# Kernel tuning notes

Hardware: AMD Instinct MI355X
Metric: run time of the kernel (lower is better)

The kernel has to match this reference:

```python
import jax, jax.numpy as jnp
import numpy as np

N_NODES = 100000
N_EDGES = 1600000
D_FEAT = 48
N_LAYERS = 3  # GCN(n_layers=3) builds exactly 3 GraphConv layers


def setup_inputs() -> dict:
    key = jax.random.key(0)
    k1, k2, k3 = jax.random.split(key, 3)
    features = jax.random.normal(k1, (N_NODES, D_FEAT), dtype=jnp.float32)
    src = jax.random.randint(k2, (N_EDGES,), 0, N_NODES, dtype=jnp.int32)
    dst = jax.random.randint(k3, (N_EDGES,), 0, N_NODES, dtype=jnp.int32)
    return {"features": features, "src": src, "dst": dst}


def reference(features, src, dst):
    # GraphConv(norm='none', weight=False, bias=False): h_v = sum_{u->v} h_u, then activation.
    # Layers 0..N_LAYERS-2 apply relu; the final layer has no activation.
    h = features
    for i in range(N_LAYERS):
        msgs = h[src]  # gather source features per edge: [E, D]
        h = jax.ops.segment_sum(msgs, dst, num_segments=N_NODES)  # scatter-add to dst
        if i < N_LAYERS - 1:
            h = jax.nn.relu(h)
    return h
```

## Files before the change

kernel.cpp:

```cpp
#include <hip/hip_runtime.h>

#define D 48
#define BSH 8
#define BN 256
#define NBMAX 400
#define CH 256
#define CAPT 5120


__global__ void k_hist(const int* __restrict__ dst, int* __restrict__ histg,
                       int E, int NB, int CHE) {
    int c = blockIdx.x;
    int t = threadIdx.x;
    __shared__ int h[NBMAX];
    for (int b = t; b < NB; b += blockDim.x) h[b] = 0;
    __syncthreads();
    int lo = c * CHE, hi = min(lo + CHE, E);
    for (int i = lo + t; i < hi; i += blockDim.x)
        atomicAdd(&h[dst[i] >> BSH], 1);
    __syncthreads();
    for (int b = t; b < NB; b += blockDim.x) histg[c * NB + b] = h[b];
}

__global__ void k_vscan(const int* __restrict__ histg, int* __restrict__ cbase,
                        int* __restrict__ btot, int NB) {
    int b = blockIdx.x;
    int t = threadIdx.x;
    __shared__ int sh[CH];
    int v = histg[t * NB + b];
    sh[t] = v;
    __syncthreads();
    for (int off = 1; off < CH; off <<= 1) {
        int u = (t >= off) ? sh[t - off] : 0;
        __syncthreads();
        sh[t] += u;
        __syncthreads();
    }
    cbase[t * NB + b] = sh[t] - v;
    if (t == CH - 1) btot[b] = sh[t];
}

__global__ void k_bscan(const int* __restrict__ btot, int* __restrict__ bbase,
                        int* __restrict__ row_ptr, int NB, int N, int E) {
    __shared__ int sh[256];
    __shared__ int srun;
    int t = threadIdx.x;
    if (t == 0) srun = 0;
    __syncthreads();
    int nch = (NB + 255) / 256;
    for (int c = 0; c < nch; c++) {
        int b = c * 256 + t;
        int v = (b < NB) ? btot[b] : 0;
        sh[t] = v;
        __syncthreads();
        for (int off = 1; off < 256; off <<= 1) {
            int u = (t >= off) ? sh[t - off] : 0;
            __syncthreads();
            sh[t] += u;
            __syncthreads();
        }
        int run = srun;
        if (b < NB) bbase[b] = run + sh[t] - v;
        __syncthreads();
        if (t == 255) srun = run + sh[255];
        __syncthreads();
    }
    if (t == 0) { bbase[NB] = E; row_ptr[N] = E; }
}

__global__ void k_scatter(const int* __restrict__ src, const int* __restrict__ dst,
                          const int* __restrict__ bbase, const int* __restrict__ cbase,
                          int* __restrict__ stage, int E, int NB, int CHE) {
    int c = blockIdx.x;
    int t = threadIdx.x;
    __shared__ int cur[NBMAX];
    for (int b = t; b < NB; b += blockDim.x)
        cur[b] = bbase[b] + cbase[c * NB + b];
    __syncthreads();
    int lo = c * CHE, hi = min(lo + CHE, E);
    for (int i = lo + t; i < hi; i += blockDim.x) {
        int s = src[i], d = dst[i];
        int p = atomicAdd(&cur[d >> BSH], 1);
        stage[p] = ((d & (BN - 1)) << 17) | s;
    }
}

__global__ void k_build(const int* __restrict__ stage, const int* __restrict__ bbase,
                        int* __restrict__ row_ptr, int* __restrict__ esrc,
                        int N, int NB) {
    int b = blockIdx.x;
    int t = threadIdx.x;
    __shared__ int lbuf[CAPT];
    __shared__ int lout[CAPT];
    __shared__ int hist[BN];
    __shared__ int cur[BN];
    __shared__ int sh[BN];
    int base = bbase[b];
    int cnt = min(bbase[b + 1] - base, CAPT);
    hist[t] = 0;
    __syncthreads();
    for (int i = t; i < cnt; i += 256) {
        int v = stage[base + i];
        lbuf[i] = v;
        atomicAdd(&hist[v >> 17], 1);
    }
    __syncthreads();
    int orig = hist[t];
    sh[t] = orig;
    __syncthreads();
    for (int off = 1; off < 256; off <<= 1) {
        int u = (t >= off) ? sh[t - off] : 0;
        __syncthreads();
        sh[t] += u;
        __syncthreads();
    }
    int excl = sh[t] - orig;
    cur[t] = excl;
    int node = (b << BSH) + t;
    if (node < N) row_ptr[node] = base + excl;
    __syncthreads();
    for (int i = t; i < cnt; i += 256) {
        int v = lbuf[i];
        int p = atomicAdd(&cur[v >> 17], 1);
        lout[p] = v & 0x1FFFF;
    }
    __syncthreads();
    for (int i = t; i < cnt; i += 256) esrc[base + i] = lout[i];
}


static __device__ inline unsigned int f2bf_rne(float x) {
    unsigned int u = __float_as_uint(x);
    return (u + 0x7FFFu + ((u >> 16) & 1u)) >> 16;
}
static __device__ inline unsigned int pack2(float lo, float hi) {
    return f2bf_rne(lo) | (f2bf_rne(hi) << 16);
}
static __device__ inline float bf_lo(unsigned int u) { return __uint_as_float(u << 16); }
static __device__ inline float bf_hi(unsigned int u) { return __uint_as_float(u & 0xFFFF0000u); }

__global__ void k_cvt(const float* __restrict__ in, unsigned int* __restrict__ out, int n4) {
    int i = blockIdx.x * 256 + threadIdx.x;
    if (i >= n4) return;
    float4 v = ((const float4*)in)[i];
    ((uint2*)out)[i] = make_uint2(pack2(v.x, v.y), pack2(v.z, v.w));
}


template <int RELU, int OUTF32>
__global__ void k_pull(const unsigned int* __restrict__ hin, void* __restrict__ hout,
                       const int* __restrict__ row_ptr, const int* __restrict__ esrc,
                       int n) {
    int grp = threadIdx.x >> 3;
    int lane = threadIdx.x & 7;
    int node = blockIdx.x * 32 + grp;
    if (node >= n) return;
    int jb = row_ptr[node], je = row_ptr[node + 1];
    float a0 = 0.f, a1 = 0.f, a2 = 0.f, a3 = 0.f, a4 = 0.f, a5 = 0.f;
    int j = jb;
    int je8 = jb + ((je - jb) & ~7);
    for (; j < je8; j += 8) {
        int s[8];
#pragma unroll
        for (int u = 0; u < 8; u++) s[u] = esrc[j + u];
        uint2 q[8];
        unsigned int w[8];
#pragma unroll
        for (int u = 0; u < 8; u++) {
            const unsigned int* r = hin + s[u] * 24;
            q[u] = *(const uint2*)(r + 2 * lane);
            w[u] = r[16 + lane];
        }
#pragma unroll
        for (int u = 0; u < 8; u++) {
            a0 += bf_lo(q[u].x); a1 += bf_hi(q[u].x);
            a2 += bf_lo(q[u].y); a3 += bf_hi(q[u].y);
            a4 += bf_lo(w[u]);   a5 += bf_hi(w[u]);
        }
    }
    if (j < je) {
        int rem = je - j;
        int s[7];
#pragma unroll
        for (int u = 0; u < 7; u++) s[u] = (u < rem) ? esrc[j + u] : s[0];
        uint2 q[7];
        unsigned int w[7];
#pragma unroll
        for (int u = 0; u < 7; u++) {
            const unsigned int* r = hin + s[u] * 24;
            if (u < rem) {
                q[u] = *(const uint2*)(r + 2 * lane);
                w[u] = r[16 + lane];
            }
        }
#pragma unroll
        for (int u = 0; u < 7; u++) {
            if (u < rem) {
                a0 += bf_lo(q[u].x); a1 += bf_hi(q[u].x);
                a2 += bf_lo(q[u].y); a3 += bf_hi(q[u].y);
                a4 += bf_lo(w[u]);   a5 += bf_hi(w[u]);
            }
        }
    }
    if (RELU) {
        a0 = fmaxf(a0, 0.f); a1 = fmaxf(a1, 0.f); a2 = fmaxf(a2, 0.f);
        a3 = fmaxf(a3, 0.f); a4 = fmaxf(a4, 0.f); a5 = fmaxf(a5, 0.f);
    }
    if (OUTF32) {
        float* o = (float*)hout + (size_t)node * D;
        *(float4*)(o + 4 * lane) = make_float4(a0, a1, a2, a3);
        *(float2*)(o + 32 + 2 * lane) = make_float2(a4, a5);
    } else {
        unsigned int* o = (unsigned int*)hout + node * 24;
        *(uint2*)(o + 2 * lane) = make_uint2(pack2(a0, a1), pack2(a2, a3));
        o[16 + lane] = pack2(a4, a5);
    }
}

extern "C" void kernel_launch(void* const* d_in, const int* in_sizes, int n_in,
                              void* d_out, int out_size, void* d_ws, size_t ws_size,
                              hipStream_t stream) {
    const float* feat = (const float*)d_in[0];
    const int* src = (const int*)d_in[1];
    const int* dst = (const int*)d_in[2];
    int N = in_sizes[0] / D;
    int E = in_sizes[1];
    int NB = (N + BN - 1) >> BSH;
    int CHE = (E + CH - 1) / CH;

    char* ws = (char*)d_ws;
    int*   histg   = (int*)(ws + ((size_t)0 << 10));
    int*   cbase   = (int*)(ws + ((size_t)512 << 10));
    int*   btot    = (int*)(ws + ((size_t)1024 << 10));
    int*   bbase   = (int*)(ws + ((size_t)1088 << 10));
    int*   row_ptr = (int*)(ws + ((size_t)2048 << 10));
    int*   esrc    = (int*)(ws + ((size_t)3 << 20));
    int*   stage   = (int*)(ws + ((size_t)10 << 20));
    unsigned int* featb = (unsigned int*)(ws + ((size_t)17 << 20));
    unsigned int* hb0   = (unsigned int*)(ws + ((size_t)27 << 20));

    k_hist<<<CH, 1024, 0, stream>>>(dst, histg, E, NB, CHE);
    k_vscan<<<NB, CH, 0, stream>>>(histg, cbase, btot, NB);
    k_bscan<<<1, 256, 0, stream>>>(btot, bbase, row_ptr, NB, N, E);
    k_scatter<<<CH, 1024, 0, stream>>>(src, dst, bbase, cbase, stage, E, NB, CHE);
    k_build<<<NB, 256, 0, stream>>>(stage, bbase, row_ptr, esrc, N, NB);

    int n4 = N * D / 4;
    k_cvt<<<(n4 + 255) / 256, 256, 0, stream>>>(feat, featb, n4);

    int pg = (N + 31) / 32;
    k_pull<1, 0><<<pg, 256, 0, stream>>>(featb, hb0, row_ptr, esrc, N);
    k_pull<1, 0><<<pg, 256, 0, stream>>>(hb0, featb, row_ptr, esrc, N);
    k_pull<0, 1><<<pg, 256, 0, stream>>>(featb, d_out, row_ptr, esrc, N);
}
```

Before: 213.5 us.

## Fuse histogram/scan/convert front end and degree-sort nodes within buckets for pull

Merges the per-chunk histogram and the vertical scan into one kernel that uses global atomics on bucket totals to hand out chunk offsets, and runs the bf16 feature conversion in extra blocks of the same launch. k_build additionally counting-sorts the nodes of each 256-node bucket by in-degree class into a perm array, and the pull kernels process nodes in that order so that groups in a wavefront see similar edge counts. The masked remainder block is replaced with a simple scalar loop. The goal is fewer launches and less divergence in the gather; the cost is an extra memset and indirection, plus chunk offsets that are no longer ordered by chunk, which still yields a correct CSR.

```diff
diff --git a/kernel.cpp b/kernel.cpp
--- a/kernel.cpp
+++ b/kernel.cpp
@@ -8,37 +8,41 @@
 #define CAPT 5120
 
 
-__global__ void k_hist(const int* __restrict__ dst, int* __restrict__ histg,
-                       int E, int NB, int CHE) {
-    int c = blockIdx.x;
-    int t = threadIdx.x;
-    __shared__ int h[NBMAX];
-    for (int b = t; b < NB; b += blockDim.x) h[b] = 0;
-    __syncthreads();
-    int lo = c * CHE, hi = min(lo + CHE, E);
-    for (int i = lo + t; i < hi; i += blockDim.x)
-        atomicAdd(&h[dst[i] >> BSH], 1);
-    __syncthreads();
-    for (int b = t; b < NB; b += blockDim.x) histg[c * NB + b] = h[b];
-}
-
-__global__ void k_vscan(const int* __restrict__ histg, int* __restrict__ cbase,
-                        int* __restrict__ btot, int NB) {
-    int b = blockIdx.x;
-    int t = threadIdx.x;
-    __shared__ int sh[CH];
-    int v = histg[t * NB + b];
-    sh[t] = v;
-    __syncthreads();
-    for (int off = 1; off < CH; off <<= 1) {
-        int u = (t >= off) ? sh[t - off] : 0;
-        __syncthreads();
-        sh[t] += u;
-        __syncthreads();
-    }
-    cbase[t * NB + b] = sh[t] - v;
-    if (t == CH - 1) btot[b] = sh[t];
-}
+static __device__ inline unsigned int f2bf_rne(float x) {
+    unsigned int u = __float_as_uint(x);
+    return (u + 0x7FFFu + ((u >> 16) & 1u)) >> 16;
+}
+static __device__ inline unsigned int pack2(float lo, float hi) {
+    return f2bf_rne(lo) | (f2bf_rne(hi) << 16);
+}
+static __device__ inline float bf_lo(unsigned int u) { return __uint_as_float(u << 16); }
+static __device__ inline float bf_hi(unsigned int u) { return __uint_as_float(u & 0xFFFF0000u); }
+
+__global__ void k_front(const int* __restrict__ dst, const float* __restrict__ feat,
+                        unsigned int* __restrict__ featb, int* __restrict__ btot,
+                        int* __restrict__ cbase, int E, int NB, int CHE, int n4) {
+    int t = threadIdx.x;
+    if (blockIdx.x < CH) {
+        int c = blockIdx.x;
+        __shared__ int h[NBMAX];
+        for (int b = t; b < NB; b += 1024) h[b] = 0;
+        __syncthreads();
+        int lo = c * CHE, hi = min(lo + CHE, E);
+        for (int i = lo + t; i < hi; i += 1024)
+            atomicAdd(&h[dst[i] >> BSH], 1);
+        __syncthreads();
+        for (int b = t; b < NB; b += 1024)
+            cbase[c * NB + b] = atomicAdd(&btot[b], h[b]);
+    } else {
+        int i = (blockIdx.x - CH) * 1024 + t;
+        int stride = 256 * 1024;
+        for (; i < n4; i += stride) {
+            float4 v = ((const float4*)feat)[i];
+            ((uint2*)featb)[i] = make_uint2(pack2(v.x, v.y), pack2(v.z, v.w));
+        }
+    }
+}
+
 
 __global__ void k_bscan(const int* __restrict__ btot, int* __restrict__ bbase,
                         int* __restrict__ row_ptr, int NB, int N, int E) {
@@ -68,6 +72,7 @@
     if (t == 0) { bbase[NB] = E; row_ptr[N] = E; }
 }
 
+
 __global__ void k_scatter(const int* __restrict__ src, const int* __restrict__ dst,
                           const int* __restrict__ bbase, const int* __restrict__ cbase,
                           int* __restrict__ stage, int E, int NB, int CHE) {
@@ -85,9 +90,10 @@
     }
 }
 
+
 __global__ void k_build(const int* __restrict__ stage, const int* __restrict__ bbase,
                         int* __restrict__ row_ptr, int* __restrict__ esrc,
-                        int N, int NB) {
+                        int* __restrict__ perm, int N, int NB) {
     int b = blockIdx.x;
     int t = threadIdx.x;
     __shared__ int lbuf[CAPT];
@@ -95,9 +101,12 @@
     __shared__ int hist[BN];
     __shared__ int cur[BN];
     __shared__ int sh[BN];
+    __shared__ int dh[64];
+    __shared__ int dcur[64];
     int base = bbase[b];
     int cnt = min(bbase[b + 1] - base, CAPT);
     hist[t] = 0;
+    if (t < 64) dh[t] = 0;
     __syncthreads();
     for (int i = t; i < cnt; i += 256) {
         int v = stage[base + i];
@@ -118,6 +127,22 @@
     cur[t] = excl;
     int node = (b << BSH) + t;
     if (node < N) row_ptr[node] = base + excl;
+    int dcls = min(orig, 63);
+    atomicAdd(&dh[dcls], 1);
+    __syncthreads();
+    if (t < 64) {
+        int v = dh[t];
+        int x = v;
+#pragma unroll
+        for (int off = 1; off < 64; off <<= 1) {
+            int u = __shfl_up(x, off);
+            if (t >= off) x += u;
+        }
+        dcur[t] = x - v;
+    }
+    __syncthreads();
+    int pos = atomicAdd(&dcur[dcls], 1);
+    perm[(b << BSH) + pos] = node;
     __syncthreads();
     for (int i = t; i < cnt; i += 256) {
         int v = lbuf[i];
@@ -129,31 +154,13 @@
 }
 
 
-static __device__ inline unsigned int f2bf_rne(float x) {
-    unsigned int u = __float_as_uint(x);
-    return (u + 0x7FFFu + ((u >> 16) & 1u)) >> 16;
-}
-static __device__ inline unsigned int pack2(float lo, float hi) {
-    return f2bf_rne(lo) | (f2bf_rne(hi) << 16);
-}
-static __device__ inline float bf_lo(unsigned int u) { return __uint_as_float(u << 16); }
-static __device__ inline float bf_hi(unsigned int u) { return __uint_as_float(u & 0xFFFF0000u); }
-
-__global__ void k_cvt(const float* __restrict__ in, unsigned int* __restrict__ out, int n4) {
-    int i = blockIdx.x * 256 + threadIdx.x;
-    if (i >= n4) return;
-    float4 v = ((const float4*)in)[i];
-    ((uint2*)out)[i] = make_uint2(pack2(v.x, v.y), pack2(v.z, v.w));
-}
-
-
 template <int RELU, int OUTF32>
 __global__ void k_pull(const unsigned int* __restrict__ hin, void* __restrict__ hout,
                        const int* __restrict__ row_ptr, const int* __restrict__ esrc,
-                       int n) {
+                       const int* __restrict__ perm, int n) {
     int grp = threadIdx.x >> 3;
     int lane = threadIdx.x & 7;
-    int node = blockIdx.x * 32 + grp;
+    int node = perm[blockIdx.x * 32 + grp];
     if (node >= n) return;
     int jb = row_ptr[node], je = row_ptr[node + 1];
     float a0 = 0.f, a1 = 0.f, a2 = 0.f, a3 = 0.f, a4 = 0.f, a5 = 0.f;
@@ -178,29 +185,14 @@
             a4 += bf_lo(w[u]);   a5 += bf_hi(w[u]);
         }
     }
-    if (j < je) {
-        int rem = je - j;
-        int s[7];
-#pragma unroll
-        for (int u = 0; u < 7; u++) s[u] = (u < rem) ? esrc[j + u] : s[0];
-        uint2 q[7];
-        unsigned int w[7];
-#pragma unroll
-        for (int u = 0; u < 7; u++) {
-            const unsigned int* r = hin + s[u] * 24;
-            if (u < rem) {
-                q[u] = *(const uint2*)(r + 2 * lane);
-                w[u] = r[16 + lane];
-            }
-        }
-#pragma unroll
-        for (int u = 0; u < 7; u++) {
-            if (u < rem) {
-                a0 += bf_lo(q[u].x); a1 += bf_hi(q[u].x);
-                a2 += bf_lo(q[u].y); a3 += bf_hi(q[u].y);
-                a4 += bf_lo(w[u]);   a5 += bf_hi(w[u]);
-            }
-        }
+    for (; j < je; ++j) {
+        int s0 = esrc[j];
+        const unsigned int* r = hin + s0 * 24;
+        uint2 q0 = *(const uint2*)(r + 2 * lane);
+        unsigned int w0 = r[16 + lane];
+        a0 += bf_lo(q0.x); a1 += bf_hi(q0.x);
+        a2 += bf_lo(q0.y); a3 += bf_hi(q0.y);
+        a4 += bf_lo(w0);   a5 += bf_hi(w0);
     }
     if (RELU) {
         a0 = fmaxf(a0, 0.f); a1 = fmaxf(a1, 0.f); a2 = fmaxf(a2, 0.f);
@@ -227,29 +219,28 @@
     int E = in_sizes[1];
     int NB = (N + BN - 1) >> BSH;
     int CHE = (E + CH - 1) / CH;
+    int n4 = N * D / 4;
 
     char* ws = (char*)d_ws;
-    int*   histg   = (int*)(ws + ((size_t)0 << 10));
-    int*   cbase   = (int*)(ws + ((size_t)512 << 10));
-    int*   btot    = (int*)(ws + ((size_t)1024 << 10));
-    int*   bbase   = (int*)(ws + ((size_t)1088 << 10));
-    int*   row_ptr = (int*)(ws + ((size_t)2048 << 10));
-    int*   esrc    = (int*)(ws + ((size_t)3 << 20));
+    int*   btot    = (int*)(ws + ((size_t)0 << 10));
+    int*   bbase   = (int*)(ws + ((size_t)64 << 10));
+    int*   cbase   = (int*)(ws + ((size_t)128 << 10));
+    int*   row_ptr = (int*)(ws + ((size_t)640 << 10));
+    int*   perm    = (int*)(ws + ((size_t)1152 << 10));
+    int*   esrc    = (int*)(ws + ((size_t)2 << 20));
     int*   stage   = (int*)(ws + ((size_t)10 << 20));
     unsigned int* featb = (unsigned int*)(ws + ((size_t)17 << 20));
     unsigned int* hb0   = (unsigned int*)(ws + ((size_t)27 << 20));
 
-    k_hist<<<CH, 1024, 0, stream>>>(dst, histg, E, NB, CHE);
-    k_vscan<<<NB, CH, 0, stream>>>(histg, cbase, btot, NB);
+    hipMemsetAsync(btot, 0, (size_t)NB * sizeof(int), stream);
+
+    k_front<<<CH + 256, 1024, 0, stream>>>(dst, feat, featb, btot, cbase, E, NB, CHE, n4);
     k_bscan<<<1, 256, 0, stream>>>(btot, bbase, row_ptr, NB, N, E);
     k_scatter<<<CH, 1024, 0, stream>>>(src, dst, bbase, cbase, stage, E, NB, CHE);
-    k_build<<<NB, 256, 0, stream>>>(stage, bbase, row_ptr, esrc, N, NB);
-
-    int n4 = N * D / 4;
-    k_cvt<<<(n4 + 255) / 256, 256, 0, stream>>>(feat, featb, n4);
-
-    int pg = (N + 31) / 32;
-    k_pull<1, 0><<<pg, 256, 0, stream>>>(featb, hb0, row_ptr, esrc, N);
-    k_pull<1, 0><<<pg, 256, 0, stream>>>(hb0, featb, row_ptr, esrc, N);
-    k_pull<0, 1><<<pg, 256, 0, stream>>>(featb, d_out, row_ptr, esrc, N);
-}
+    k_build<<<NB, 256, 0, stream>>>(stage, bbase, row_ptr, esrc, perm, N, NB);
+
+    int pg = NB * 8;
+    k_pull<1, 0><<<pg, 256, 0, stream>>>(featb, hb0, row_ptr, esrc, perm, N);
+    k_pull<1, 0><<<pg, 256, 0, stream>>>(hb0, featb, row_ptr, esrc, perm, N);
+    k_pull<0, 1><<<pg, 256, 0, stream>>>(featb, d_out, row_ptr, esrc, perm, N);
+}
```

After: 252.9 us. +18.5%, slower.
